# Kernel optimization log

Hardware: AMD Instinct MI355X
Metric: run time of the kernel (lower is better)

Reference implementation:

```python
import jax, jax.numpy as jnp
import numpy as np

DIM = 1024
HEADS = 8
DIM_HEAD = 64
INNER = HEADS * DIM_HEAD  # 512
SCALE = 8.0


def l2norm(t, eps=1e-12):
    # matches F.normalize(t, dim=-1)
    n = jnp.linalg.norm(t, axis=-1, keepdims=True)
    return t / jnp.maximum(n, eps)


def setup_inputs() -> dict:
    key = jax.random.key(0)
    ks = jax.random.split(key, 5)
    x = jax.random.normal(ks[0], (4, 2048, DIM), dtype=jnp.float32)
    # torch Linear weights are [out, in]; store transposed [in, out] for x @ W
    s = 1.0 / np.sqrt(DIM)
    Wq = jax.random.uniform(ks[1], (DIM, INNER), jnp.float32, -s, s)
    Wk = jax.random.uniform(ks[2], (DIM, INNER), jnp.float32, -s, s)
    Wv = jax.random.uniform(ks[3], (DIM, INNER), jnp.float32, -s, s)
    so = 1.0 / np.sqrt(INNER)
    Wo = jax.random.uniform(ks[4], (INNER, DIM), jnp.float32, -so, so)
    return {"x": x, "Wq": Wq, "Wk": Wk, "Wv": Wv, "Wo": Wo}


def reference(x, Wq, Wk, Wv, Wo):
    b, n, _ = x.shape
    def split_heads(t):
        return t.reshape(b, n, HEADS, DIM_HEAD).transpose(0, 2, 1, 3)  # b h n d
    q = split_heads(x @ Wq)
    k = split_heads(x @ Wk)
    v = split_heads(x @ Wv)
    # cosine-sim attention: l2-normalize q, k then fixed scale
    q = l2norm(q)
    k = l2norm(k)
    sim = jnp.einsum('bhid,bhjd->bhij', q, k) * SCALE
    causal_mask = jnp.triu(jnp.ones((n, n), dtype=bool), k=1)
    sim = jnp.where(causal_mask, jnp.finfo(sim.dtype).min, sim)
    attn = jax.nn.softmax(sim, axis=-1)
    o = jnp.einsum('bhij,bhjd->bhid', attn, v)
    o = o.transpose(0, 2, 1, 3).reshape(b, n, INNER)
    return o @ Wo
```

## Files before the change

### kernel.cpp

```cpp
#include <hip/hip_runtime.h>
#include <hip/hip_bf16.h>

typedef __attribute__((ext_vector_type(8))) __bf16 bf16x8;
typedef __attribute__((ext_vector_type(4))) __bf16 bf16x4;
typedef __attribute__((ext_vector_type(4))) float f32x4;

#define MFMA16(a, b, c) __builtin_amdgcn_mfma_f32_16x16x32_bf16(a, b, c, 0, 0, 0)

static __device__ __forceinline__ ushort f2b(float f) {
    __bf16 b = (__bf16)f;
    return __builtin_bit_cast(ushort, b);
}
static __device__ __forceinline__ bf16x8 cat44(bf16x4 a, bf16x4 b) {
    bf16x8 r;
    r[0] = a[0]; r[1] = a[1]; r[2] = a[2]; r[3] = a[3];
    r[4] = b[0]; r[5] = b[1]; r[6] = b[2]; r[7] = b[3];
    return r;
}
static __device__ __forceinline__ void gload_lds16(const ushort* g, ushort* l) {
    __builtin_amdgcn_global_load_lds(
        (const __attribute__((address_space(1))) unsigned int*)g,
        (__attribute__((address_space(3))) unsigned int*)l, 16, 0, 0);
}
static __device__ __forceinline__ float exp2_fast(float x) {
    float r;
    asm("v_exp_f32 %0, %1" : "=v"(r) : "v"(x));
    return r;
}

__global__ void f32_to_bf16_k(const float* __restrict__ in, ushort* __restrict__ out, int n4) {
    int i = blockIdx.x * blockDim.x + threadIdx.x;
    if (i >= n4) return;
    float4 v = reinterpret_cast<const float4*>(in)[i];
    ushort4 o;
    o.x = f2b(v.x); o.y = f2b(v.y); o.z = f2b(v.z); o.w = f2b(v.w);
    reinterpret_cast<ushort4*>(out)[i] = o;
}

__global__ __launch_bounds__(256)
void transpose_all_k(const float* __restrict__ Wq, const float* __restrict__ Wk,
                     const float* __restrict__ Wv, const float* __restrict__ Wo,
                     ushort* __restrict__ Wqkv, ushort* __restrict__ Wot) {
    __shared__ ushort T[64][72];
    const int bid = blockIdx.x;
    const int job = bid >> 7;
    const int t = bid & 127;
    const float* src; ushort* dst; int K, N;
    if (job == 0)      { src = Wq; dst = Wqkv;                      K = 1024; N = 512; }
    else if (job == 1) { src = Wk; dst = Wqkv + (size_t)512 * 1024; K = 1024; N = 512; }
    else if (job == 2) { src = Wv; dst = Wqkv + (size_t)1024 * 1024; K = 1024; N = 512; }
    else               { src = Wo; dst = Wot;                       K = 512;  N = 1024; }
    const int tn = N >> 6;
    const int bk = t / tn, bn = t - bk * tn;
    const int k0 = bk * 64, n0 = bn * 64;
    const int tid = threadIdx.x;
#pragma unroll
    for (int q = 0; q < 4; ++q) {
        const int lin = tid + 256 * q;
        const int kr = lin >> 4;
        const int n4 = (lin & 15) << 2;
        float4 v = *reinterpret_cast<const float4*>(&src[(size_t)(k0 + kr) * N + n0 + n4]);
        T[n4 + 0][kr] = f2b(v.x);
        T[n4 + 1][kr] = f2b(v.y);
        T[n4 + 2][kr] = f2b(v.z);
        T[n4 + 3][kr] = f2b(v.w);
    }
    __syncthreads();
#pragma unroll
    for (int s = 0; s < 2; ++s) {
        const int lin = tid + 256 * s;
        const int n = lin >> 3;
        const int kc = (lin & 7) << 3;
        ushort4 a, b;
        a.x = T[n][kc + 0]; a.y = T[n][kc + 1]; a.z = T[n][kc + 2]; a.w = T[n][kc + 3];
        b.x = T[n][kc + 4]; b.y = T[n][kc + 5]; b.z = T[n][kc + 6]; b.w = T[n][kc + 7];
        ushort* p = &dst[(size_t)(n0 + n) * K + k0 + kc];
        *reinterpret_cast<ushort4*>(p) = a;
        *reinterpret_cast<ushort4*>(p + 4) = b;
    }
}

template <int F32OUT, int ROUTE>
__global__ __launch_bounds__(256)
void gemm_tile_k(const ushort* __restrict__ A, const ushort* __restrict__ Bt,
                 void* __restrict__ C0, void* __restrict__ C1, void* __restrict__ C2,
                 int M, int N, int K, int nby) {
    __shared__ __align__(16) ushort As[128 * 32];
    __shared__ __align__(16) ushort Bs[128 * 32];
    const int tid = threadIdx.x;
    const int lane = tid & 63;
    const int w = tid >> 6;
    const int l15 = lane & 15, g = lane >> 4;
    const int wr = w >> 1, wc = w & 1;

    const int nwg = gridDim.x;
    const int cpx = nwg >> 3;
    const int bid = blockIdx.x;
    const int swz = (bid & 7) * cpx + (bid >> 3);
    const int bx = swz / nby, by = swz - bx * nby;
    const int rbase = bx * 128, cbase = by * 128;

    const int srow = lane >> 2;
    const int scol = (lane & 3) * 8;
    const ushort* Aw0 = A + (size_t)(rbase + 32 * w + srow) * K + scol;
    const ushort* Bw0 = Bt + (size_t)(cbase + 32 * w + srow) * K + scol;

    f32x4 acc[4][4];
#pragma unroll
    for (int m = 0; m < 4; ++m)
#pragma unroll
        for (int n = 0; n < 4; ++n) acc[m][n] = (f32x4){0, 0, 0, 0};

    const int nk = K >> 5;
    for (int kt = 0; kt < nk; ++kt) {
        const int k0 = kt << 5;
        if (kt) __syncthreads();
        gload_lds16(Aw0 + k0,          &As[(32 * w) * 32]);
        gload_lds16(Aw0 + 16 * K + k0, &As[(32 * w + 16) * 32]);
        gload_lds16(Bw0 + k0,          &Bs[(32 * w) * 32]);
        gload_lds16(Bw0 + 16 * K + k0, &Bs[(32 * w + 16) * 32]);
        __syncthreads();
        bf16x8 af[4], bf[4];
#pragma unroll
        for (int m = 0; m < 4; ++m)
            af[m] = *reinterpret_cast<const bf16x8*>(&As[(64 * wr + 16 * m + l15) * 32 + 8 * g]);
#pragma unroll
        for (int n = 0; n < 4; ++n)
            bf[n] = *reinterpret_cast<const bf16x8*>(&Bs[(64 * wc + 16 * n + l15) * 32 + 8 * g]);
#pragma unroll
        for (int m = 0; m < 4; ++m)
#pragma unroll
            for (int n = 0; n < 4; ++n)
                acc[m][n] = MFMA16(af[m], bf[n], acc[m][n]);
    }

    if (ROUTE) {
        const int col0 = cbase + 64 * wc;
        const int grp = col0 >> 9;
        const int co0 = col0 & 511;
        if (grp == 2) {
            const int h = co0 >> 6;
#pragma unroll
            for (int m = 0; m < 4; ++m) {
                const int row = rbase + 64 * wr + 16 * m + 4 * g;
                const int bb = row >> 11;
                const int tok = row & 2047;
#pragma unroll
                for (int n = 0; n < 4; ++n) {
                    const int d = 16 * n + l15;
                    bf16x4 wv;
#pragma unroll
                    for (int r = 0; r < 4; ++r) wv[r] = (__bf16)acc[m][n][r];
                    ushort* dst = (ushort*)C2 + (((size_t)(bb * 8 + h) * 64 + d) * 2048 + tok);
                    *reinterpret_cast<bf16x4*>(dst) = wv;
                }
            }
        } else {
            ushort* Cg = (ushort*)(grp == 0 ? C0 : C1);
#pragma unroll
            for (int m = 0; m < 4; ++m) {
                f32x4 ss = {0, 0, 0, 0};
#pragma unroll
                for (int n = 0; n < 4; ++n)
#pragma unroll
                    for (int r = 0; r < 4; ++r) ss[r] += acc[m][n][r] * acc[m][n][r];
#pragma unroll
                for (int r = 0; r < 4; ++r) {
                    float s = ss[r];
                    s += __shfl_xor(s, 1);
                    s += __shfl_xor(s, 2);
                    s += __shfl_xor(s, 4);
                    s += __shfl_xor(s, 8);
                    ss[r] = 1.0f / fmaxf(sqrtf(s), 1e-12f);
                }
                const int row = rbase + 64 * wr + 16 * m + 4 * g;
#pragma unroll
                for (int n = 0; n < 4; ++n) {
                    const int co = co0 + 16 * n + l15;
#pragma unroll
                    for (int r = 0; r < 4; ++r)
                        Cg[(size_t)(row + r) * 512 + co] = f2b(acc[m][n][r] * ss[r]);
                }
            }
        }
    } else {
#pragma unroll
        for (int m = 0; m < 4; ++m)
#pragma unroll
            for (int n = 0; n < 4; ++n) {
                const int row = rbase + 64 * wr + 16 * m + 4 * g;
                const int col = cbase + 64 * wc + 16 * n + l15;
                if (F32OUT) {
#pragma unroll
                    for (int r = 0; r < 4; ++r)
                        reinterpret_cast<float*>(C0)[(size_t)(row + r) * N + col] = acc[m][n][r];
                } else {
#pragma unroll
                    for (int r = 0; r < 4; ++r)
                        reinterpret_cast<ushort*>(C0)[(size_t)(row + r) * N + col] = f2b(acc[m][n][r]);
                }
            }
    }
}

__global__ __launch_bounds__(128, 2)
void flash_attn_k(const ushort* __restrict__ Q, const ushort* __restrict__ K,
                  const ushort* __restrict__ Vt, ushort* __restrict__ O) {
    __shared__ __align__(16) ushort Ks[64 * 64];
    __shared__ __align__(16) ushort Vs[64 * 64];
    const int tid = threadIdx.x;
    const int lane = tid & 63;
    const int wave = tid >> 6;
    const int l15 = lane & 15;
    const int g = lane >> 4;
    const int bh = blockIdx.x;
    const int b = bh >> 3, h = bh & 7;
    const int j = blockIdx.y;
    const int ytrue = (j < 16) ? j : 47 - j;
    const int wglob = ytrue * 2 + wave;
    const int c0 = wglob;
    const int c1 = 127 - wglob;
    const int q0 = c0 * 16 + l15;
    const int q1 = c1 * 16 + l15;
    const int nt0 = (c0 * 16 + 79) >> 6;
    const int nt1 = (c1 * 16 + 79) >> 6;
    const int ntb = ((127 - 2 * ytrue) * 16 + 79) >> 6;

    const float CEXP = 11.5415603f;

    const ushort* Qb = Q + (size_t)(b * 2048) * 512 + h * 64;
    const ushort* Kb = K + (size_t)(b * 2048) * 512 + h * 64;
    const ushort* Vb = Vt + (size_t)bh * 64 * 2048;

    const ushort* kSrc[4];
    const ushort* vSrc[4];
    ushort* kDst[4];
    ushort* vDst[4];
#pragma unroll
    for (int i = 0; i < 4; ++i) {
        const int s = tid + 128 * i;
        const int row = s >> 3;
        const int cc = s & 7;
        const int sc = cc ^ (row & 7);
        kSrc[i] = Kb + (size_t)row * 512 + sc * 8;
        vSrc[i] = Vb + (size_t)row * 2048 + sc * 8;
        const int base = (wave * 64 + 128 * i) * 8;
        kDst[i] = &Ks[base];
        vDst[i] = &Vs[base];
    }

    bf16x8 qf0[2], qf1[2];
#pragma unroll
    for (int kh = 0; kh < 2; ++kh) {
        qf0[kh] = *reinterpret_cast<const bf16x8*>(Qb + (size_t)q0 * 512 + 32 * kh + 8 * g);
        qf1[kh] = *reinterpret_cast<const bf16x8*>(Qb + (size_t)q1 * 512 + 32 * kh + 8 * g);
    }

    bf16x8 ones;
#pragma unroll
    for (int i = 0; i < 8; ++i) ones[i] = (__bf16)1.0f;

    f32x4 acc0[4], acc1[4];
#pragma unroll
    for (int d = 0; d < 4; ++d) {
        acc0[d] = (f32x4){0, 0, 0, 0};
        acc1[d] = (f32x4){0, 0, 0, 0};
    }
    f32x4 lac0 = {0, 0, 0, 0}, lac1 = {0, 0, 0, 0};

    for (int t = 0; t < ntb; ++t) {
        if (t) __syncthreads();
#pragma unroll
        for (int i = 0; i < 4; ++i) gload_lds16(kSrc[i] + (size_t)t * 32768, kDst[i]);
#pragma unroll
        for (int i = 0; i < 4; ++i) gload_lds16(vSrc[i] + t * 64, vDst[i]);
        __syncthreads();

        if (t >= nt1) continue;
        const bool act0 = (t < nt0);
        const bool mk0 = (t == nt0 - 1);
        const bool mk1 = (t == nt1 - 1);

        bf16x8 af[4][2];
#pragma unroll
        for (int jt = 0; jt < 4; ++jt)
#pragma unroll
            for (int kh = 0; kh < 2; ++kh) {
                const int row = jt * 16 + l15;
                const int chunk = (g + 4 * kh) ^ (row & 7);
                af[jt][kh] = *reinterpret_cast<const bf16x8*>(&Ks[row * 64 + chunk * 8]);
            }
        bf16x4 vf[4][2][2];
#pragma unroll
        for (int d = 0; d < 4; ++d)
#pragma unroll
            for (int kk = 0; kk < 2; ++kk)
#pragma unroll
                for (int th = 0; th < 2; ++th) {
                    const int dr = d * 16 + l15;
                    const int chunk = ((g >> 1) + 2 * th + 4 * kk) ^ (dr & 7);
                    vf[d][kk][th] = *reinterpret_cast<const bf16x4*>(
                        &Vs[dr * 64 + chunk * 8 + (g & 1) * 4]);
                }

        f32x4 s1[4], s0[4];
#pragma unroll
        for (int jt = 0; jt < 4; ++jt) {
            f32x4 z = {0, 0, 0, 0};
            z = MFMA16(af[jt][0], qf1[0], z);
            s1[jt] = MFMA16(af[jt][1], qf1[1], z);
        }
        if (act0) {
#pragma unroll
            for (int jt = 0; jt < 4; ++jt) {
                f32x4 z = {0, 0, 0, 0};
                z = MFMA16(af[jt][0], qf0[0], z);
                s0[jt] = MFMA16(af[jt][1], qf0[1], z);
            }
        }

        bf16x8 pt1[2];
#pragma unroll
        for (int jt = 0; jt < 4; ++jt) {
#pragma unroll
            for (int r = 0; r < 4; ++r) {
                float p = exp2_fast(fmaf(s1[jt][r], CEXP, -CEXP));
                if (mk1) {
                    int jj = t * 64 + jt * 16 + 4 * g + r;
                    p = (jj <= q1) ? p : 0.0f;
                }
                pt1[jt >> 1][(jt & 1) * 4 + r] = (__bf16)p;
            }
        }

        __builtin_amdgcn_s_setprio(1);
#pragma unroll
        for (int d = 0; d < 4; ++d) {
            bf16x8 v0 = cat44(vf[d][0][0], vf[d][0][1]);
            bf16x8 v1 = cat44(vf[d][1][0], vf[d][1][1]);
            acc1[d] = MFMA16(v0, pt1[0], acc1[d]);
            acc1[d] = MFMA16(v1, pt1[1], acc1[d]);
        }
        lac1 = MFMA16(ones, pt1[0], lac1);
        lac1 = MFMA16(ones, pt1[1], lac1);
        __builtin_amdgcn_s_setprio(0);

        if (act0) {
            bf16x8 pt0[2];
#pragma unroll
            for (int jt = 0; jt < 4; ++jt) {
#pragma unroll
                for (int r = 0; r < 4; ++r) {
                    float p = exp2_fast(fmaf(s0[jt][r], CEXP, -CEXP));
                    if (mk0) {
                        int jj = t * 64 + jt * 16 + 4 * g + r;
                        p = (jj <= q0) ? p : 0.0f;
                    }
                    pt0[jt >> 1][(jt & 1) * 4 + r] = (__bf16)p;
                }
            }
            __builtin_amdgcn_s_setprio(1);
#pragma unroll
            for (int d = 0; d < 4; ++d) {
                bf16x8 v0 = cat44(vf[d][0][0], vf[d][0][1]);
                bf16x8 v1 = cat44(vf[d][1][0], vf[d][1][1]);
                acc0[d] = MFMA16(v0, pt0[0], acc0[d]);
                acc0[d] = MFMA16(v1, pt0[1], acc0[d]);
            }
            lac0 = MFMA16(ones, pt0[0], lac0);
            lac0 = MFMA16(ones, pt0[1], lac0);
            __builtin_amdgcn_s_setprio(0);
        }
    }

    auto fin = [&](f32x4 (&acc)[4], float ls, int qr) {
        float inv = 1.0f / ls;
        ushort* Ob = O + (size_t)(b * 2048 + qr) * 512 + h * 64;
#pragma unroll
        for (int d = 0; d < 4; ++d) {
            bf16x4 w;
#pragma unroll
            for (int r = 0; r < 4; ++r) w[r] = (__bf16)(acc[d][r] * inv);
            *reinterpret_cast<bf16x4*>(Ob + d * 16 + 4 * g) = w;
        }
    };
    fin(acc1, lac1[0], q1);
    fin(acc0, lac0[0], q0);
}

extern "C" void kernel_launch(void* const* d_in, const int* in_sizes, int n_in,
                              void* d_out, int out_size, void* d_ws, size_t ws_size,
                              hipStream_t stream) {
    const float* x  = (const float*)d_in[0];
    const float* Wq = (const float*)d_in[1];
    const float* Wk = (const float*)d_in[2];
    const float* Wv = (const float*)d_in[3];
    const float* Wo = (const float*)d_in[4];
    float* out = (float*)d_out;

    char* ws = (char*)d_ws;
    ushort* xb  = (ushort*)ws; ws += (size_t)8192 * 1024 * 2;
    ushort* Wqt = (ushort*)ws; ws += (size_t)1536 * 1024 * 2;
    ushort* Wot = (ushort*)ws; ws += (size_t)1024 * 512 * 2;
    ushort* Qm  = (ushort*)ws; ws += (size_t)8192 * 512 * 2;
    ushort* Km  = (ushort*)ws; ws += (size_t)8192 * 512 * 2;
    ushort* Vtm = (ushort*)ws; ws += (size_t)8192 * 512 * 2;
    ushort* Om  = xb;

    f32_to_bf16_k<<<8192, 256, 0, stream>>>(x, xb, 2097152);
    transpose_all_k<<<512, 256, 0, stream>>>(Wq, Wk, Wv, Wo, Wqt, Wot);

    gemm_tile_k<0, 1><<<768, 256, 0, stream>>>(xb, Wqt, Qm, Km, Vtm, 8192, 1536, 1024, 12);

    flash_attn_k<<<dim3(32, 32), 128, 0, stream>>>(Qm, Km, Vtm, Om);

    gemm_tile_k<1, 0><<<512, 256, 0, stream>>>(Om, Wot, out, nullptr, nullptr, 8192, 1024, 512, 8);
}
```

Baseline: 109.1 us.

## Split attention KV range across two wave-halves and merge partial sums

Doubles the attention block to 256 threads so that two wave pairs process disjoint halves of the key/value tile range for the same query rows, each with its own LDS staging buffers. The partial accumulators and row sums are combined through shared memory at the end. This works because the cosine-sim scores are bounded, so the softmax needs no running max. The aim is to shorten the serial KV loop per block and raise the number of waves in flight. The cost is extra LDS, a final reduction with two extra barriers, and idle waves in the upper half for short rows.

```diff
diff --git a/kernel.cpp b/kernel.cpp
--- a/kernel.cpp
+++ b/kernel.cpp
@@ -203,21 +203,22 @@
     }
 }
 
-__global__ __launch_bounds__(128, 2)
+__global__ __launch_bounds__(256, 4)
 void flash_attn_k(const ushort* __restrict__ Q, const ushort* __restrict__ K,
-                  const ushort* __restrict__ Vt, ushort* __restrict__ O) {
-    __shared__ __align__(16) ushort Ks[64 * 64];
-    __shared__ __align__(16) ushort Vs[64 * 64];
+                  const ushort* __restrict__ Vg, ushort* __restrict__ O) {
+    __shared__ __align__(16) ushort S[4][4096];
     const int tid = threadIdx.x;
     const int lane = tid & 63;
     const int wave = tid >> 6;
+    const int half = wave >> 1;
+    const int wsel = wave & 1;
     const int l15 = lane & 15;
     const int g = lane >> 4;
     const int bh = blockIdx.x;
     const int b = bh >> 3, h = bh & 7;
     const int j = blockIdx.y;
     const int ytrue = (j < 16) ? j : 47 - j;
-    const int wglob = ytrue * 2 + wave;
+    const int wglob = ytrue * 2 + wsel;
     const int c0 = wglob;
     const int c1 = 127 - wglob;
     const int q0 = c0 * 16 + l15;
@@ -225,28 +226,21 @@
     const int nt0 = (c0 * 16 + 79) >> 6;
     const int nt1 = (c1 * 16 + 79) >> 6;
     const int ntb = ((127 - 2 * ytrue) * 16 + 79) >> 6;
+    const int mid = (ntb + 1) >> 1;
+    const int tbase = half ? mid : 0;
 
     const float CEXP = 11.5415603f;
 
     const ushort* Qb = Q + (size_t)(b * 2048) * 512 + h * 64;
     const ushort* Kb = K + (size_t)(b * 2048) * 512 + h * 64;
-    const ushort* Vb = Vt + (size_t)bh * 64 * 2048;
-
-    const ushort* kSrc[4];
-    const ushort* vSrc[4];
-    ushort* kDst[4];
-    ushort* vDst[4];
-#pragma unroll
-    for (int i = 0; i < 4; ++i) {
-        const int s = tid + 128 * i;
-        const int row = s >> 3;
-        const int cc = s & 7;
-        const int sc = cc ^ (row & 7);
-        kSrc[i] = Kb + (size_t)row * 512 + sc * 8;
-        vSrc[i] = Vb + (size_t)row * 2048 + sc * 8;
-        const int base = (wave * 64 + 128 * i) * 8;
-        kDst[i] = &Ks[base];
-        vDst[i] = &Vs[base];
+    const ushort* Vb = Vg + (size_t)bh * 64 * 2048;
+
+    int srow[2], ssc[2];
+#pragma unroll
+    for (int i = 0; i < 2; ++i) {
+        const int s = tid + 256 * i;
+        srow[i] = s >> 3;
+        ssc[i] = (s & 7) ^ (srow[i] & 7);
     }
 
     bf16x8 qf0[2], qf1[2];
@@ -268,14 +262,28 @@
     }
     f32x4 lac0 = {0, 0, 0, 0}, lac1 = {0, 0, 0, 0};
 
-    for (int t = 0; t < ntb; ++t) {
-        if (t) __syncthreads();
-#pragma unroll
-        for (int i = 0; i < 4; ++i) gload_lds16(kSrc[i] + (size_t)t * 32768, kDst[i]);
-#pragma unroll
-        for (int i = 0; i < 4; ++i) gload_lds16(vSrc[i] + t * 64, vDst[i]);
+    const ushort* Kt = S[half * 2];
+    const ushort* Vt = S[half * 2 + 1];
+
+    for (int s = 0; s < mid; ++s) {
+        if (s) __syncthreads();
+#pragma unroll
+        for (int i = 0; i < 2; ++i) {
+            const int sl = tid + 256 * i;
+            gload_lds16(Kb + (size_t)(s * 64 + srow[i]) * 512 + ssc[i] * 8, &S[0][sl * 8]);
+            gload_lds16(Vb + (size_t)srow[i] * 2048 + s * 64 + ssc[i] * 8, &S[1][sl * 8]);
+        }
+        if (mid + s < ntb) {
+#pragma unroll
+            for (int i = 0; i < 2; ++i) {
+                const int sl = tid + 256 * i;
+                gload_lds16(Kb + (size_t)((mid + s) * 64 + srow[i]) * 512 + ssc[i] * 8, &S[2][sl * 8]);
+                gload_lds16(Vb + (size_t)srow[i] * 2048 + (mid + s) * 64 + ssc[i] * 8, &S[3][sl * 8]);
+            }
+        }
         __syncthreads();
 
+        const int t = tbase + s;
         if (t >= nt1) continue;
         const bool act0 = (t < nt0);
         const bool mk0 = (t == nt0 - 1);
@@ -288,7 +296,7 @@
             for (int kh = 0; kh < 2; ++kh) {
                 const int row = jt * 16 + l15;
                 const int chunk = (g + 4 * kh) ^ (row & 7);
-                af[jt][kh] = *reinterpret_cast<const bf16x8*>(&Ks[row * 64 + chunk * 8]);
+                af[jt][kh] = *reinterpret_cast<const bf16x8*>(&Kt[row * 64 + chunk * 8]);
             }
         bf16x4 vf[4][2][2];
 #pragma unroll
@@ -300,7 +308,7 @@
                     const int dr = d * 16 + l15;
                     const int chunk = ((g >> 1) + 2 * th + 4 * kk) ^ (dr & 7);
                     vf[d][kk][th] = *reinterpret_cast<const bf16x4*>(
-                        &Vs[dr * 64 + chunk * 8 + (g & 1) * 4]);
+                        &Vt[dr * 64 + chunk * 8 + (g & 1) * 4]);
                 }
 
         f32x4 s1[4], s0[4];
@@ -373,19 +381,50 @@
         }
     }
 
-    auto fin = [&](f32x4 (&acc)[4], float ls, int qr) {
-        float inv = 1.0f / ls;
-        ushort* Ob = O + (size_t)(b * 2048 + qr) * 512 + h * 64;
-#pragma unroll
-        for (int d = 0; d < 4; ++d) {
-            bf16x4 w;
-#pragma unroll
-            for (int r = 0; r < 4; ++r) w[r] = (__bf16)(acc[d][r] * inv);
-            *reinterpret_cast<bf16x4*>(Ob + d * 16 + 4 * g) = w;
-        }
-    };
-    fin(acc1, lac1[0], q1);
-    fin(acc0, lac0[0], q0);
+    __syncthreads();
+    if (half == 1) {
+        float* dst = (float*)S[wsel * 2];
+#pragma unroll
+        for (int d = 0; d < 4; ++d)
+#pragma unroll
+            for (int r = 0; r < 4; ++r) {
+                dst[(d * 4 + r) * 64 + lane] = acc1[d][r];
+                dst[1024 + (d * 4 + r) * 64 + lane] = acc0[d][r];
+            }
+        if (g == 0) {
+            float* lf = (float*)S[1];
+            lf = (float*)S[3];
+            lf[wsel * 32 + l15] = lac1[0];
+            lf[wsel * 32 + 16 + l15] = lac0[0];
+        }
+    }
+    __syncthreads();
+    if (half == 0) {
+        const float* src = (const float*)S[wsel * 2];
+        const float* lf = (const float*)S[3];
+        const float l1 = lac1[0] + lf[wsel * 32 + l15];
+        const float l0 = lac0[0] + lf[wsel * 32 + 16 + l15];
+#pragma unroll
+        for (int d = 0; d < 4; ++d)
+#pragma unroll
+            for (int r = 0; r < 4; ++r) {
+                acc1[d][r] += src[(d * 4 + r) * 64 + lane];
+                acc0[d][r] += src[1024 + (d * 4 + r) * 64 + lane];
+            }
+        auto fin = [&](f32x4 (&acc)[4], float ls, int qr) {
+            float inv = 1.0f / ls;
+            ushort* Ob = O + (size_t)(b * 2048 + qr) * 512 + h * 64;
+#pragma unroll
+            for (int d = 0; d < 4; ++d) {
+                bf16x4 w;
+#pragma unroll
+                for (int r = 0; r < 4; ++r) w[r] = (__bf16)(acc[d][r] * inv);
+                *reinterpret_cast<bf16x4*>(Ob + d * 16 + 4 * g) = w;
+            }
+        };
+        fin(acc1, l1, q1);
+        fin(acc0, l0, q0);
+    }
 }
 
 extern "C" void kernel_launch(void* const* d_in, const int* in_sizes, int n_in,
@@ -412,7 +451,7 @@
 
     gemm_tile_k<0, 1><<<768, 256, 0, stream>>>(xb, Wqt, Qm, Km, Vtm, 8192, 1536, 1024, 12);
 
-    flash_attn_k<<<dim3(32, 32), 128, 0, stream>>>(Qm, Km, Vtm, Om);
+    flash_attn_k<<<dim3(32, 32), 256, 0, stream>>>(Qm, Km, Vtm, Om);
 
     gemm_tile_k<1, 0><<<512, 256, 0, stream>>>(Om, Wot, out, nullptr, nullptr, 8192, 1024, 512, 8);
 }
```

After: 185.4 us. 69.9% more time.

## Fuse input prep kernels and widen GEMM K-tile to 64 with swizzled LDS

Applied to the files above, without the earlier changes.

Merges the x-to-bf16 conversion and weight transpose into one launch, removing a kernel launch and its gap. The GEMM now stages a 64-wide K slice per iteration instead of 32, halving the number of barrier-separated iterations. It uses an XOR swizzle on LDS chunks to avoid bank conflicts on fragment reads. LDS use doubles to 32KB per block, which may reduce occupancy.

```diff
diff --git a/kernel.cpp b/kernel.cpp
--- a/kernel.cpp
+++ b/kernel.cpp
@@ -28,32 +28,33 @@
     return r;
 }
 
-__global__ void f32_to_bf16_k(const float* __restrict__ in, ushort* __restrict__ out, int n4) {
-    int i = blockIdx.x * blockDim.x + threadIdx.x;
-    if (i >= n4) return;
-    float4 v = reinterpret_cast<const float4*>(in)[i];
-    ushort4 o;
-    o.x = f2b(v.x); o.y = f2b(v.y); o.z = f2b(v.z); o.w = f2b(v.w);
-    reinterpret_cast<ushort4*>(out)[i] = o;
-}
-
 __global__ __launch_bounds__(256)
-void transpose_all_k(const float* __restrict__ Wq, const float* __restrict__ Wk,
-                     const float* __restrict__ Wv, const float* __restrict__ Wo,
-                     ushort* __restrict__ Wqkv, ushort* __restrict__ Wot) {
+void prep_k(const float* __restrict__ x, ushort* __restrict__ xb,
+            const float* __restrict__ Wq, const float* __restrict__ Wk,
+            const float* __restrict__ Wv, const float* __restrict__ Wo,
+            ushort* __restrict__ Wqkv, ushort* __restrict__ Wot) {
+    const int bid = blockIdx.x;
+    const int tid = threadIdx.x;
+    if (bid < 8192) {
+        int i = bid * 256 + tid;
+        float4 v = reinterpret_cast<const float4*>(x)[i];
+        ushort4 o;
+        o.x = f2b(v.x); o.y = f2b(v.y); o.z = f2b(v.z); o.w = f2b(v.w);
+        reinterpret_cast<ushort4*>(xb)[i] = o;
+        return;
+    }
     __shared__ ushort T[64][72];
-    const int bid = blockIdx.x;
-    const int job = bid >> 7;
-    const int t = bid & 127;
+    const int bb = bid - 8192;
+    const int job = bb >> 7;
+    const int t = bb & 127;
     const float* src; ushort* dst; int K, N;
-    if (job == 0)      { src = Wq; dst = Wqkv;                      K = 1024; N = 512; }
-    else if (job == 1) { src = Wk; dst = Wqkv + (size_t)512 * 1024; K = 1024; N = 512; }
+    if (job == 0)      { src = Wq; dst = Wqkv;                       K = 1024; N = 512; }
+    else if (job == 1) { src = Wk; dst = Wqkv + (size_t)512 * 1024;  K = 1024; N = 512; }
     else if (job == 2) { src = Wv; dst = Wqkv + (size_t)1024 * 1024; K = 1024; N = 512; }
-    else               { src = Wo; dst = Wot;                       K = 512;  N = 1024; }
+    else               { src = Wo; dst = Wot;                        K = 512;  N = 1024; }
     const int tn = N >> 6;
     const int bk = t / tn, bn = t - bk * tn;
     const int k0 = bk * 64, n0 = bn * 64;
-    const int tid = threadIdx.x;
 #pragma unroll
     for (int q = 0; q < 4; ++q) {
         const int lin = tid + 256 * q;
@@ -85,8 +86,8 @@
 void gemm_tile_k(const ushort* __restrict__ A, const ushort* __restrict__ Bt,
                  void* __restrict__ C0, void* __restrict__ C1, void* __restrict__ C2,
                  int M, int N, int K, int nby) {
-    __shared__ __align__(16) ushort As[128 * 32];
-    __shared__ __align__(16) ushort Bs[128 * 32];
+    __shared__ __align__(16) ushort As[128 * 64];
+    __shared__ __align__(16) ushort Bs[128 * 64];
     const int tid = threadIdx.x;
     const int lane = tid & 63;
     const int w = tid >> 6;
@@ -100,10 +101,12 @@
     const int bx = swz / nby, by = swz - bx * nby;
     const int rbase = bx * 128, cbase = by * 128;
 
-    const int srow = lane >> 2;
-    const int scol = (lane & 3) * 8;
-    const ushort* Aw0 = A + (size_t)(rbase + 32 * w + srow) * K + scol;
-    const ushort* Bw0 = Bt + (size_t)(cbase + 32 * w + srow) * K + scol;
+    const int lr = lane >> 3;
+    const int sc = (lane & 7) ^ lr;
+    const ushort* Ap = A + (size_t)(rbase + 32 * w + lr) * K + sc * 8;
+    const ushort* Bp = Bt + (size_t)(cbase + 32 * w + lr) * K + sc * 8;
+    ushort* AsD = &As[(32 * w) * 64];
+    ushort* BsD = &Bs[(32 * w) * 64];
 
     f32x4 acc[4][4];
 #pragma unroll
@@ -111,27 +114,42 @@
 #pragma unroll
         for (int n = 0; n < 4; ++n) acc[m][n] = (f32x4){0, 0, 0, 0};
 
-    const int nk = K >> 5;
+    const int nk = K >> 6;
     for (int kt = 0; kt < nk; ++kt) {
-        const int k0 = kt << 5;
+        const int k0 = kt << 6;
         if (kt) __syncthreads();
-        gload_lds16(Aw0 + k0,          &As[(32 * w) * 32]);
-        gload_lds16(Aw0 + 16 * K + k0, &As[(32 * w + 16) * 32]);
-        gload_lds16(Bw0 + k0,          &Bs[(32 * w) * 32]);
-        gload_lds16(Bw0 + 16 * K + k0, &Bs[(32 * w + 16) * 32]);
+#pragma unroll
+        for (int i = 0; i < 4; ++i) {
+            gload_lds16(Ap + (size_t)(8 * i) * K + k0, AsD + (8 * i) * 64);
+            gload_lds16(Bp + (size_t)(8 * i) * K + k0, BsD + (8 * i) * 64);
+        }
         __syncthreads();
-        bf16x8 af[4], bf[4];
+        bf16x8 af[4][2], bfr[4][2];
+#pragma unroll
+        for (int m = 0; m < 4; ++m) {
+            const int row = 64 * wr + 16 * m + l15;
+#pragma unroll
+            for (int kh = 0; kh < 2; ++kh) {
+                const int ch = (g + 4 * kh) ^ (l15 & 7);
+                af[m][kh] = *reinterpret_cast<const bf16x8*>(&As[row * 64 + ch * 8]);
+            }
+        }
+#pragma unroll
+        for (int n = 0; n < 4; ++n) {
+            const int row = 64 * wc + 16 * n + l15;
+#pragma unroll
+            for (int kh = 0; kh < 2; ++kh) {
+                const int ch = (g + 4 * kh) ^ (l15 & 7);
+                bfr[n][kh] = *reinterpret_cast<const bf16x8*>(&Bs[row * 64 + ch * 8]);
+            }
+        }
 #pragma unroll
         for (int m = 0; m < 4; ++m)
-            af[m] = *reinterpret_cast<const bf16x8*>(&As[(64 * wr + 16 * m + l15) * 32 + 8 * g]);
-#pragma unroll
-        for (int n = 0; n < 4; ++n)
-            bf[n] = *reinterpret_cast<const bf16x8*>(&Bs[(64 * wc + 16 * n + l15) * 32 + 8 * g]);
-#pragma unroll
-        for (int m = 0; m < 4; ++m)
-#pragma unroll
-            for (int n = 0; n < 4; ++n)
-                acc[m][n] = MFMA16(af[m], bf[n], acc[m][n]);
+#pragma unroll
+            for (int n = 0; n < 4; ++n) {
+                acc[m][n] = MFMA16(af[m][0], bfr[n][0], acc[m][n]);
+                acc[m][n] = MFMA16(af[m][1], bfr[n][1], acc[m][n]);
+            }
     }
 
     if (ROUTE) {
@@ -241,9 +259,9 @@
         const int s = tid + 128 * i;
         const int row = s >> 3;
         const int cc = s & 7;
-        const int sc = cc ^ (row & 7);
-        kSrc[i] = Kb + (size_t)row * 512 + sc * 8;
-        vSrc[i] = Vb + (size_t)row * 2048 + sc * 8;
+        const int scc = cc ^ (row & 7);
+        kSrc[i] = Kb + (size_t)row * 512 + scc * 8;
+        vSrc[i] = Vb + (size_t)row * 2048 + scc * 8;
         const int base = (wave * 64 + 128 * i) * 8;
         kDst[i] = &Ks[base];
         vDst[i] = &Vs[base];
@@ -407,8 +425,7 @@
     ushort* Vtm = (ushort*)ws; ws += (size_t)8192 * 512 * 2;
     ushort* Om  = xb;
 
-    f32_to_bf16_k<<<8192, 256, 0, stream>>>(x, xb, 2097152);
-    transpose_all_k<<<512, 256, 0, stream>>>(Wq, Wk, Wv, Wo, Wqt, Wot);
+    prep_k<<<8704, 256, 0, stream>>>(x, xb, Wq, Wk, Wv, Wo, Wqt, Wot);
 
     gemm_tile_k<0, 1><<<768, 256, 0, stream>>>(xb, Wqt, Qm, Km, Vtm, 8192, 1536, 1024, 12);
 
```

Result: no change. 110.6 us (+1.3%).
